# Performance work log

Measured on AMD Instinct MI355X. Metric: run time of the kernel, lower is better.

## Reference

```python
import jax, jax.numpy as jnp
import numpy as np

N, T, I_TEXT, H, P = 64, 1024, 512, 512, 256


def setup_inputs() -> dict:
    key = jax.random.key(0)
    ks = jax.random.split(key, 7)
    s = 0.05  # keep recurrent dynamics stable
    return {
        "text_encoding": jax.random.normal(ks[0], (N, T, I_TEXT), jnp.float32),
        "text_lengths": jnp.full((N,), T, dtype=jnp.int32),
        "W_ih": jax.random.normal(ks[1], (3 * H, I_TEXT + P), jnp.float32) * s,
        "W_hh": jax.random.normal(ks[2], (3 * H, H), jnp.float32) * s,
        "b_ih": jax.random.normal(ks[3], (3 * H,), jnp.float32) * s,
        "b_hh": jax.random.normal(ks[4], (3 * H,), jnp.float32) * s,
        "W_p": jax.random.normal(ks[5], (P, H), jnp.float32) * s,
        "b_p": jax.random.normal(ks[6], (P,), jnp.float32) * s,
    }


def reference(text_encoding, text_lengths, W_ih, W_hh, b_ih, b_hh, W_p, b_p):
    n, t, _ = text_encoding.shape
    h_dim = W_hh.shape[1]
    p_dim = W_p.shape[0]
    xs = jnp.transpose(text_encoding, (1, 0, 2))  # [T, N, I_text]

    def step(carry, x):
        h, prev = carry  # h: [N,H] GRU hidden, prev: [N,P] last projected prosody vec
        inp = jnp.concatenate([x, prev], axis=-1)          # [N, I_text+P]
        gi = inp @ W_ih.T + b_ih                           # [N, 3H]
        gh = h @ W_hh.T + b_hh                             # [N, 3H]
        i_r, i_z, i_n = jnp.split(gi, 3, axis=-1)
        h_r, h_z, h_n = jnp.split(gh, 3, axis=-1)
        r = jax.nn.sigmoid(i_r + h_r)
        z = jax.nn.sigmoid(i_z + h_z)
        g = jnp.tanh(i_n + r * h_n)
        h_new = (1.0 - z) * g + z * h
        pred = h_new @ W_p.T + b_p                         # [N, P]
        return (h_new, pred), pred

    h0 = jnp.zeros((n, h_dim), text_encoding.dtype)
    p0 = jnp.zeros((n, p_dim), text_encoding.dtype)
    _, preds = jax.lax.scan(step, (h0, p0), xs)            # [T, N, P]
    return jnp.transpose(preds, (1, 0, 2))                 # [N, T, P]
```

## Files before the change

kernel.cpp:

```cpp
#include <hip/hip_runtime.h>
#include <hip/hip_bf16.h>


typedef short short8 __attribute__((ext_vector_type(8)));
typedef float f32x4 __attribute__((ext_vector_type(4)));

__device__ __forceinline__ unsigned short f2bf(float f) {
  __hip_bfloat16 h = __float2bfloat16(f);
  return *reinterpret_cast<unsigned short*>(&h);
}

__global__ void k_zero(unsigned int* __restrict__ p, int n) {
  int i = blockIdx.x * 256 + threadIdx.x;
  if (i < n) p[i] = 0u;
}

__global__ void k_fold(const float* __restrict__ W_ih, const float* __restrict__ W_hh,
                       const float* __restrict__ W_p, const float* __restrict__ b_p,
                       float* __restrict__ W_big, float* __restrict__ v_bp) {
  int idx = blockIdx.x * 256 + threadIdx.x;
  int i = idx >> 9;
  int j = idx & 511;
  const float* wip = W_ih + (long)i * 768 + 512;
  float q = 0.f;
  for (int k = 0; k < 256; ++k) q = fmaf(wip[k], W_p[k * 512 + j], q);
  if (i < 1024) {
    W_big[(long)i * 512 + j] = W_hh[(long)i * 512 + j] + q;
  } else {
    W_big[(long)i * 512 + j] = q;
    W_big[(long)(i + 512) * 512 + j] = W_hh[(long)i * 512 + j];
  }
  if (j == 0) {
    float s = 0.f;
    for (int k = 0; k < 256; ++k) s = fmaf(b_p[k], wip[k], s);
    v_bp[i] = s;
  }
}

__global__ void k_pack(const float* __restrict__ W_big, const float* __restrict__ W_ih,
                       const float* __restrict__ W_p,
                       unsigned short* __restrict__ Wr, unsigned short* __restrict__ Wx) {
  long e = (long)blockIdx.x * 256 + threadIdx.x;
  if (e < 1572864) {
    int k = (int)(e & 511);
    int cc = (int)((e >> 9) & 15);
    int rest = (int)(e >> 13);
    int T = rest % 3, b = rest / 3;
    int j = b * 8 + (cc & 7);
    bool hi = cc >= 8;
    float v;
    if (T == 0)      v = W_big[(long)(hi ? 512 + j : j) * 512 + k];
    else if (T == 1) v = W_big[(long)(hi ? 1536 + j : 1024 + j) * 512 + k];
    else             v = (cc < 4) ? W_p[(long)(b * 4 + cc) * 512 + k] : 0.f;
    Wr[e] = f2bf(v);
  } else {
    long e2 = e - 1572864;
    int k = (int)(e2 & 511);
    int cc = (int)((e2 >> 9) & 15);
    int rest = (int)(e2 >> 13);
    int T = rest & 1, b = rest >> 1;
    float v = 0.f;
    if (T == 0) {
      int row = (cc < 8) ? (b * 8 + cc) : (512 + b * 8 + (cc - 8));
      v = W_ih[(long)row * 768 + k];
    } else if (cc < 8) {
      v = W_ih[(long)(1024 + b * 8 + cc) * 768 + k];
    }
    Wx[e2] = f2bf(v);
  }
}

__global__ __launch_bounds__(256, 1) void k_persist(
    const float* __restrict__ x,
    const unsigned short* __restrict__ Wr, const unsigned short* __restrict__ Wxr,
    const float* __restrict__ b_ih, const float* __restrict__ b_hh,
    const float* __restrict__ v_bp, const float* __restrict__ b_p,
    unsigned short* __restrict__ Hbf,
    float* __restrict__ out,
    unsigned int* __restrict__ flags,
    unsigned int* __restrict__ dead) {
  const int tid = threadIdx.x;
  const int b = blockIdx.x;
  const int w = tid >> 6, lane = tid & 63, c = lane & 15, q = lane >> 4;
  const int j0 = b * 8, n0 = w * 16, jj = j0 + (c & 7), pcol = b * 4 + (c & 3);

  __shared__ unsigned short wxl[32 * 528];

  short8 wr0[16], wr1[16], wr2[16];
#pragma unroll
  for (int ki = 0; ki < 16; ++ki) {
    wr0[ki] = *(const short8*)(Wr + (((long)(b * 3 + 0) * 16 + c) * 512 + ki * 32 + q * 8));
    wr1[ki] = *(const short8*)(Wr + (((long)(b * 3 + 1) * 16 + c) * 512 + ki * 32 + q * 8));
    wr2[ki] = *(const short8*)(Wr + (((long)(b * 3 + 2) * 16 + c) * 512 + ki * 32 + q * 8));
  }
  {
    const unsigned short* src = Wxr + (long)b * 16384;
    int row = tid >> 3, ch = tid & 7;
#pragma unroll
    for (int i = 0; i < 8; ++i) {
      int col = ch * 64 + i * 8;
      *(short8*)&wxl[row * 528 + col] = *(const short8*)(src + row * 512 + col);
    }
  }

  const float bihr = b_ih[jj],        bhhr = b_hh[jj],        vbr = v_bp[jj];
  const float bihz = b_ih[512 + jj],  bhhz = b_hh[512 + jj],  vbz = v_bp[512 + jj];
  const float bihn = b_ih[1024 + jj], bhhn = b_hh[1024 + jj], vbn = v_bp[1024 + jj];
  const float bp = b_p[pcol];
  float hprev[4] = {0.f, 0.f, 0.f, 0.f};
  f32x4 gp0{0.f, 0.f, 0.f, 0.f}, gp1 = gp0;
  bool alive = true;

  __syncthreads();

  auto produce = [&](int tt) {
    f32x4 p0{0.f, 0.f, 0.f, 0.f}, p1 = p0;
    const float* xr = x + ((long)(n0 + c) * 1024 + tt) * 512 + q * 8;
#pragma unroll
    for (int ki = 0; ki < 16; ++ki) {
      float4 f0 = *(const float4*)(xr + ki * 32);
      float4 f1 = *(const float4*)(xr + ki * 32 + 4);
      short8 ax;
      ax[0] = f2bf(f0.x); ax[1] = f2bf(f0.y); ax[2] = f2bf(f0.z); ax[3] = f2bf(f0.w);
      ax[4] = f2bf(f1.x); ax[5] = f2bf(f1.y); ax[6] = f2bf(f1.z); ax[7] = f2bf(f1.w);
      short8 b0 = *(const short8*)&wxl[c * 528 + ki * 32 + q * 8];
      short8 b1 = *(const short8*)&wxl[(16 + c) * 528 + ki * 32 + q * 8];
      p0 = __builtin_amdgcn_mfma_f32_16x16x32_bf16(ax, b0, p0, 0, 0, 0);
      p1 = __builtin_amdgcn_mfma_f32_16x16x32_bf16(ax, b1, p1, 0, 0, 0);
    }
    gp0 = p0; gp1 = p1;
  };

  produce(0);

  for (int t = 0; t <= 1024; ++t) {
    const int cur = t & 1;
    const unsigned short* hb = Hbf + (long)cur * 32768 + (long)(n0 + c) * 512 + q * 8;
    short8 h0, h1, h2, h3, h4, h5, h6, h7, h8, h9, hA, hB, hC, hD, hE, hF;
    asm volatile(
        "global_load_dwordx4 %[o0], %[a], off sc0 sc1\n\t"
        "global_load_dwordx4 %[o1], %[a], off offset:64 sc0 sc1\n\t"
        "global_load_dwordx4 %[o2], %[a], off offset:128 sc0 sc1\n\t"
        "global_load_dwordx4 %[o3], %[a], off offset:192 sc0 sc1\n\t"
        "global_load_dwordx4 %[o4], %[a], off offset:256 sc0 sc1\n\t"
        "global_load_dwordx4 %[o5], %[a], off offset:320 sc0 sc1\n\t"
        "global_load_dwordx4 %[o6], %[a], off offset:384 sc0 sc1\n\t"
        "global_load_dwordx4 %[o7], %[a], off offset:448 sc0 sc1\n\t"
        "global_load_dwordx4 %[o8], %[a], off offset:512 sc0 sc1\n\t"
        "global_load_dwordx4 %[o9], %[a], off offset:576 sc0 sc1\n\t"
        "global_load_dwordx4 %[oA], %[a], off offset:640 sc0 sc1\n\t"
        "global_load_dwordx4 %[oB], %[a], off offset:704 sc0 sc1\n\t"
        "global_load_dwordx4 %[oC], %[a], off offset:768 sc0 sc1\n\t"
        "global_load_dwordx4 %[oD], %[a], off offset:832 sc0 sc1\n\t"
        "global_load_dwordx4 %[oE], %[a], off offset:896 sc0 sc1\n\t"
        "global_load_dwordx4 %[oF], %[a], off offset:960 sc0 sc1\n\t"
        "s_waitcnt vmcnt(0)"
        : [o0]"=&v"(h0), [o1]"=&v"(h1), [o2]"=&v"(h2), [o3]"=&v"(h3),
          [o4]"=&v"(h4), [o5]"=&v"(h5), [o6]"=&v"(h6), [o7]"=&v"(h7),
          [o8]"=&v"(h8), [o9]"=&v"(h9), [oA]"=&v"(hA), [oB]"=&v"(hB),
          [oC]"=&v"(hC), [oD]"=&v"(hD), [oE]"=&v"(hE), [oF]"=&v"(hF)
        : [a]"v"(hb)
        : "memory");

    f32x4 a0{0.f, 0.f, 0.f, 0.f}, a1 = a0, a2 = a0;
#define RK(H, K)                                                          \
    a0 = __builtin_amdgcn_mfma_f32_16x16x32_bf16(H, wr0[K], a0, 0, 0, 0); \
    a1 = __builtin_amdgcn_mfma_f32_16x16x32_bf16(H, wr1[K], a1, 0, 0, 0); \
    a2 = __builtin_amdgcn_mfma_f32_16x16x32_bf16(H, wr2[K], a2, 0, 0, 0);
    RK(h0, 0)  RK(h1, 1)  RK(h2, 2)  RK(h3, 3)
    RK(h4, 4)  RK(h5, 5)  RK(h6, 6)  RK(h7, 7)
    RK(h8, 8)  RK(h9, 9)  RK(hA, 10) RK(hB, 11)
    RK(hC, 12) RK(hD, 13) RK(hE, 14) RK(hF, 15)
#undef RK

    if (t >= 1 && c < 4) {
#pragma unroll
      for (int r = 0; r < 4; ++r)
        out[((long)(n0 + q * 4 + r) * 1024 + (t - 1)) * 256 + pcol] = a2[r] + bp;
    }
    if (t == 1024) break;

    const float cR = t ? (bihr + bhhr + vbr) : (bihr + bhhr);
    const float cZ = t ? (bihz + bhhz + vbz) : (bihz + bhhz);
    const float cN = t ? (bihn + vbn) : bihn;
    float s0x[4], s1x[4];
#pragma unroll
    for (int r = 0; r < 4; ++r) { s0x[r] = a0[r] + gp0[r]; s1x[r] = a1[r] + gp1[r]; }
    unsigned short* hw = Hbf + (long)(cur ^ 1) * 32768 + (long)(n0 + q * 4) * 512 + jj;
#pragma unroll
    for (int r = 0; r < 4; ++r) {
      float ps0 = __shfl_xor(s0x[r], 8);
      float ps1 = __shfl_xor(s1x[r], 8);
      if (c < 8) {
        float rr = __builtin_amdgcn_rcpf(1.f + __expf(-(s0x[r] + cR)));
        float zz = __builtin_amdgcn_rcpf(1.f + __expf(-(ps0 + cZ)));
        float aa = s1x[r] + cN + rr * (ps1 + bhhn);
        float gg = 1.f - 2.f * __builtin_amdgcn_rcpf(1.f + __expf(2.f * aa));
        float hn = (1.f - zz) * gg + zz * hprev[r];
        hprev[r] = hn;
        unsigned short hv = f2bf(hn);
        unsigned short* pr = hw + r * 512;
        asm volatile("global_store_short %0, %1, off sc0 sc1" :: "v"(pr), "v"(hv) : "memory");
      }
    }

    asm volatile("s_waitcnt vmcnt(0)" ::: "memory");
    __syncthreads();
    const unsigned int rnd = (unsigned int)t + 1u;
    if (tid == 0 && alive)
      __hip_atomic_store(&flags[b * 16], rnd, __ATOMIC_RELAXED, __HIP_MEMORY_SCOPE_AGENT);

    if (t < 1023) produce(t + 1);

    if (tid < 64 && alive) {
      int spins = 0;
      while (__hip_atomic_load(&flags[tid * 16], __ATOMIC_RELAXED,
                               __HIP_MEMORY_SCOPE_AGENT) < rnd) {
        __builtin_amdgcn_s_sleep(1);
        if ((++spins & 2047) == 0) {
          if (__hip_atomic_load(dead, __ATOMIC_RELAXED, __HIP_MEMORY_SCOPE_AGENT)) {
            alive = false; break;
          }
          if (spins > 1000000) {
            __hip_atomic_store(dead, 1u, __ATOMIC_RELAXED, __HIP_MEMORY_SCOPE_AGENT);
            alive = false; break;
          }
        }
      }
    }
    __syncthreads();
  }
}

extern "C" void kernel_launch(void* const* d_in, const int* in_sizes, int n_in,
                              void* d_out, int out_size, void* d_ws, size_t ws_size,
                              hipStream_t stream) {
  const float* x    = (const float*)d_in[0];
  const float* W_ih = (const float*)d_in[2];
  const float* W_hh = (const float*)d_in[3];
  const float* b_ih = (const float*)d_in[4];
  const float* b_hh = (const float*)d_in[5];
  const float* W_p  = (const float*)d_in[6];
  const float* b_p  = (const float*)d_in[7];
  float* out = (float*)d_out;

  constexpr size_t OFF_WBIG = 0;
  constexpr size_t OFF_VBP  = 4194304;
  constexpr size_t OFF_WR   = 4202496;
  constexpr size_t OFF_WXR  = 7348224;
  constexpr size_t OFF_HBF  = 9445376;
  constexpr size_t OFF_FLG  = 9576448;
  constexpr size_t OFF_DEAD = 9580544;
  constexpr size_t WS_NEED  = 9580608;
  if (ws_size < WS_NEED) return;

  char* ws = (char*)d_ws;
  float* W_big        = (float*)(ws + OFF_WBIG);
  float* v_bp         = (float*)(ws + OFF_VBP);
  unsigned short* Wr  = (unsigned short*)(ws + OFF_WR);
  unsigned short* Wxr = (unsigned short*)(ws + OFF_WXR);
  unsigned short* Hbf = (unsigned short*)(ws + OFF_HBF);
  unsigned int* flags = (unsigned int*)(ws + OFF_FLG);
  unsigned int* dead  = (unsigned int*)(ws + OFF_DEAD);

  k_zero<<<133, 256, 0, stream>>>((unsigned int*)(ws + OFF_HBF), 33808);
  k_fold<<<3072, 256, 0, stream>>>(W_ih, W_hh, W_p, b_p, W_big, v_bp);
  k_pack<<<10240, 256, 0, stream>>>(W_big, W_ih, W_p, Wr, Wxr);
  k_persist<<<64, 256, 0, stream>>>(x, Wr, Wxr, b_ih, b_hh, v_bp, b_p,
                                    Hbf, out, flags, dead);
}
```

Baseline: 13.03 ms.

## Replace grid flag barrier with per-element step-tagged hidden state polling

The global barrier (block flag store, per-block spin on all flags, two __syncthreads) is removed. Each hidden-state element is now stored as a 32-bit word carrying the step number in its upper 16 bits next to the bf16 value. Consumers poll their own hidden-state loads until every tag matches the current step, then repack the words into bf16 MFMA operands. This drops barrier latency and lets blocks proceed as soon as their data is ready, at the cost of doubling hidden-state traffic, adding repacking work, and relying on ordering of the dword stores.

```diff
diff --git a/kernel.cpp b/kernel.cpp
--- a/kernel.cpp
+++ b/kernel.cpp
@@ -4,6 +4,7 @@
 
 typedef short short8 __attribute__((ext_vector_type(8)));
 typedef float f32x4 __attribute__((ext_vector_type(4)));
+typedef unsigned int u32x4 __attribute__((ext_vector_type(4)));
 
 __device__ __forceinline__ unsigned short f2bf(float f) {
   __hip_bfloat16 h = __float2bfloat16(f);
@@ -75,9 +76,8 @@
     const unsigned short* __restrict__ Wr, const unsigned short* __restrict__ Wxr,
     const float* __restrict__ b_ih, const float* __restrict__ b_hh,
     const float* __restrict__ v_bp, const float* __restrict__ b_p,
-    unsigned short* __restrict__ Hbf,
+    unsigned int* __restrict__ Hd,
     float* __restrict__ out,
-    unsigned int* __restrict__ flags,
     unsigned int* __restrict__ dead) {
   const int tid = threadIdx.x;
   const int b = blockIdx.x;
@@ -133,45 +133,81 @@
 
   produce(0);
 
+#define LOAD16(BASE)                                                        \
+  asm volatile(                                                             \
+      "global_load_dwordx4 %[o0], %[a], off sc0 sc1\n\t"                    \
+      "global_load_dwordx4 %[o1], %[a], off offset:16 sc0 sc1\n\t"          \
+      "global_load_dwordx4 %[o2], %[a], off offset:128 sc0 sc1\n\t"         \
+      "global_load_dwordx4 %[o3], %[a], off offset:144 sc0 sc1\n\t"         \
+      "global_load_dwordx4 %[o4], %[a], off offset:256 sc0 sc1\n\t"         \
+      "global_load_dwordx4 %[o5], %[a], off offset:272 sc0 sc1\n\t"         \
+      "global_load_dwordx4 %[o6], %[a], off offset:384 sc0 sc1\n\t"         \
+      "global_load_dwordx4 %[o7], %[a], off offset:400 sc0 sc1\n\t"         \
+      "global_load_dwordx4 %[o8], %[a], off offset:512 sc0 sc1\n\t"         \
+      "global_load_dwordx4 %[o9], %[a], off offset:528 sc0 sc1\n\t"         \
+      "global_load_dwordx4 %[oA], %[a], off offset:640 sc0 sc1\n\t"         \
+      "global_load_dwordx4 %[oB], %[a], off offset:656 sc0 sc1\n\t"         \
+      "global_load_dwordx4 %[oC], %[a], off offset:768 sc0 sc1\n\t"         \
+      "global_load_dwordx4 %[oD], %[a], off offset:784 sc0 sc1\n\t"         \
+      "global_load_dwordx4 %[oE], %[a], off offset:896 sc0 sc1\n\t"         \
+      "global_load_dwordx4 %[oF], %[a], off offset:912 sc0 sc1\n\t"         \
+      "s_waitcnt vmcnt(0)"                                                  \
+      : [o0]"=&v"(d0), [o1]"=&v"(d1), [o2]"=&v"(d2), [o3]"=&v"(d3),         \
+        [o4]"=&v"(d4), [o5]"=&v"(d5), [o6]"=&v"(d6), [o7]"=&v"(d7),         \
+        [o8]"=&v"(d8), [o9]"=&v"(d9), [oA]"=&v"(dA), [oB]"=&v"(dB),         \
+        [oC]"=&v"(dC), [oD]"=&v"(dD), [oE]"=&v"(dE), [oF]"=&v"(dF)          \
+      : [a]"v"(BASE)                                                        \
+      : "memory")
+
+#define ORT(DD) acc |= (DD.x ^ texp) | (DD.y ^ texp) | (DD.z ^ texp) | (DD.w ^ texp)
+
+#define POLL16(BASE)                                                        \
+  { int spins = 0;                                                          \
+    for (;;) {                                                              \
+      LOAD16(BASE);                                                         \
+      unsigned int acc = 0;                                                 \
+      ORT(d0); ORT(d1); ORT(d2); ORT(d3); ORT(d4); ORT(d5); ORT(d6); ORT(d7);\
+      ORT(d8); ORT(d9); ORT(dA); ORT(dB); ORT(dC); ORT(dD); ORT(dE); ORT(dF);\
+      if (!__any((int)(acc >> 16))) break;                                  \
+      if ((++spins & 63) == 0) {                                            \
+        if (__hip_atomic_load(dead, __ATOMIC_RELAXED, __HIP_MEMORY_SCOPE_AGENT)) { \
+          alive = false; break;                                             \
+        }                                                                   \
+        if (spins > 200000) {                                               \
+          __hip_atomic_store(dead, 1u, __ATOMIC_RELAXED, __HIP_MEMORY_SCOPE_AGENT); \
+          alive = false; break;                                             \
+        }                                                                   \
+      }                                                                     \
+    }                                                                       \
+  }
+
+#define PACK2(HI, LO) __builtin_amdgcn_perm((HI), (LO), 0x05040100u)
+#define PKMFMA(DA, DB, K)                                                   \
+  { u32x4 pw;                                                               \
+    pw.x = PACK2(DA.y, DA.x); pw.y = PACK2(DA.w, DA.z);                     \
+    pw.z = PACK2(DB.y, DB.x); pw.w = PACK2(DB.w, DB.z);                     \
+    short8 ah = __builtin_bit_cast(short8, pw);                             \
+    a0 = __builtin_amdgcn_mfma_f32_16x16x32_bf16(ah, wr0[K], a0, 0, 0, 0);  \
+    a1 = __builtin_amdgcn_mfma_f32_16x16x32_bf16(ah, wr1[K], a1, 0, 0, 0);  \
+    a2 = __builtin_amdgcn_mfma_f32_16x16x32_bf16(ah, wr2[K], a2, 0, 0, 0); }
+
   for (int t = 0; t <= 1024; ++t) {
     const int cur = t & 1;
-    const unsigned short* hb = Hbf + (long)cur * 32768 + (long)(n0 + c) * 512 + q * 8;
-    short8 h0, h1, h2, h3, h4, h5, h6, h7, h8, h9, hA, hB, hC, hD, hE, hF;
-    asm volatile(
-        "global_load_dwordx4 %[o0], %[a], off sc0 sc1\n\t"
-        "global_load_dwordx4 %[o1], %[a], off offset:64 sc0 sc1\n\t"
-        "global_load_dwordx4 %[o2], %[a], off offset:128 sc0 sc1\n\t"
-        "global_load_dwordx4 %[o3], %[a], off offset:192 sc0 sc1\n\t"
-        "global_load_dwordx4 %[o4], %[a], off offset:256 sc0 sc1\n\t"
-        "global_load_dwordx4 %[o5], %[a], off offset:320 sc0 sc1\n\t"
-        "global_load_dwordx4 %[o6], %[a], off offset:384 sc0 sc1\n\t"
-        "global_load_dwordx4 %[o7], %[a], off offset:448 sc0 sc1\n\t"
-        "global_load_dwordx4 %[o8], %[a], off offset:512 sc0 sc1\n\t"
-        "global_load_dwordx4 %[o9], %[a], off offset:576 sc0 sc1\n\t"
-        "global_load_dwordx4 %[oA], %[a], off offset:640 sc0 sc1\n\t"
-        "global_load_dwordx4 %[oB], %[a], off offset:704 sc0 sc1\n\t"
-        "global_load_dwordx4 %[oC], %[a], off offset:768 sc0 sc1\n\t"
-        "global_load_dwordx4 %[oD], %[a], off offset:832 sc0 sc1\n\t"
-        "global_load_dwordx4 %[oE], %[a], off offset:896 sc0 sc1\n\t"
-        "global_load_dwordx4 %[oF], %[a], off offset:960 sc0 sc1\n\t"
-        "s_waitcnt vmcnt(0)"
-        : [o0]"=&v"(h0), [o1]"=&v"(h1), [o2]"=&v"(h2), [o3]"=&v"(h3),
-          [o4]"=&v"(h4), [o5]"=&v"(h5), [o6]"=&v"(h6), [o7]"=&v"(h7),
-          [o8]"=&v"(h8), [o9]"=&v"(h9), [oA]"=&v"(hA), [oB]"=&v"(hB),
-          [oC]"=&v"(hC), [oD]"=&v"(hD), [oE]"=&v"(hE), [oF]"=&v"(hF)
-        : [a]"v"(hb)
-        : "memory");
+    const unsigned int texp = ((unsigned int)t) << 16;
+    const unsigned int* hp = Hd + (long)cur * 32768 + (long)(n0 + c) * 512 + q * 8;
 
     f32x4 a0{0.f, 0.f, 0.f, 0.f}, a1 = a0, a2 = a0;
-#define RK(H, K)                                                          \
-    a0 = __builtin_amdgcn_mfma_f32_16x16x32_bf16(H, wr0[K], a0, 0, 0, 0); \
-    a1 = __builtin_amdgcn_mfma_f32_16x16x32_bf16(H, wr1[K], a1, 0, 0, 0); \
-    a2 = __builtin_amdgcn_mfma_f32_16x16x32_bf16(H, wr2[K], a2, 0, 0, 0);
-    RK(h0, 0)  RK(h1, 1)  RK(h2, 2)  RK(h3, 3)
-    RK(h4, 4)  RK(h5, 5)  RK(h6, 6)  RK(h7, 7)
-    RK(h8, 8)  RK(h9, 9)  RK(hA, 10) RK(hB, 11)
-    RK(hC, 12) RK(hD, 13) RK(hE, 14) RK(hF, 15)
-#undef RK
+    u32x4 d0, d1, d2, d3, d4, d5, d6, d7, d8, d9, dA, dB, dC, dD, dE, dF;
+
+    POLL16(hp);
+    if (!alive) break;
+    PKMFMA(d0, d1, 0)  PKMFMA(d2, d3, 1)  PKMFMA(d4, d5, 2)  PKMFMA(d6, d7, 3)
+    PKMFMA(d8, d9, 4)  PKMFMA(dA, dB, 5)  PKMFMA(dC, dD, 6)  PKMFMA(dE, dF, 7)
+
+    POLL16(hp + 256);
+    if (!alive) break;
+    PKMFMA(d0, d1, 8)  PKMFMA(d2, d3, 9)  PKMFMA(d4, d5, 10) PKMFMA(d6, d7, 11)
+    PKMFMA(d8, d9, 12) PKMFMA(dA, dB, 13) PKMFMA(dC, dD, 14) PKMFMA(dE, dF, 15)
 
     if (t >= 1 && c < 4) {
 #pragma unroll
@@ -186,7 +222,8 @@
     float s0x[4], s1x[4];
 #pragma unroll
     for (int r = 0; r < 4; ++r) { s0x[r] = a0[r] + gp0[r]; s1x[r] = a1[r] + gp1[r]; }
-    unsigned short* hw = Hbf + (long)(cur ^ 1) * 32768 + (long)(n0 + q * 4) * 512 + jj;
+    unsigned int* hw = Hd + (long)(cur ^ 1) * 32768 + (long)(n0 + q * 4) * 512 + jj;
+    const unsigned int tg = ((unsigned int)(t + 1)) << 16;
 #pragma unroll
     for (int r = 0; r < 4; ++r) {
       float ps0 = __shfl_xor(s0x[r], 8);
@@ -198,38 +235,18 @@
         float gg = 1.f - 2.f * __builtin_amdgcn_rcpf(1.f + __expf(2.f * aa));
         float hn = (1.f - zz) * gg + zz * hprev[r];
         hprev[r] = hn;
-        unsigned short hv = f2bf(hn);
-        unsigned short* pr = hw + r * 512;
-        asm volatile("global_store_short %0, %1, off sc0 sc1" :: "v"(pr), "v"(hv) : "memory");
+        unsigned int hv = tg | (unsigned int)f2bf(hn);
+        const unsigned int* pr = hw + r * 512;
+        asm volatile("global_store_dword %0, %1, off sc0 sc1" :: "v"(pr), "v"(hv) : "memory");
       }
     }
-
-    asm volatile("s_waitcnt vmcnt(0)" ::: "memory");
-    __syncthreads();
-    const unsigned int rnd = (unsigned int)t + 1u;
-    if (tid == 0 && alive)
-      __hip_atomic_store(&flags[b * 16], rnd, __ATOMIC_RELAXED, __HIP_MEMORY_SCOPE_AGENT);
-
     if (t < 1023) produce(t + 1);
-
-    if (tid < 64 && alive) {
-      int spins = 0;
-      while (__hip_atomic_load(&flags[tid * 16], __ATOMIC_RELAXED,
-                               __HIP_MEMORY_SCOPE_AGENT) < rnd) {
-        __builtin_amdgcn_s_sleep(1);
-        if ((++spins & 2047) == 0) {
-          if (__hip_atomic_load(dead, __ATOMIC_RELAXED, __HIP_MEMORY_SCOPE_AGENT)) {
-            alive = false; break;
-          }
-          if (spins > 1000000) {
-            __hip_atomic_store(dead, 1u, __ATOMIC_RELAXED, __HIP_MEMORY_SCOPE_AGENT);
-            alive = false; break;
-          }
-        }
-      }
-    }
-    __syncthreads();
-  }
+  }
+#undef LOAD16
+#undef ORT
+#undef POLL16
+#undef PACK2
+#undef PKMFMA
 }
 
 extern "C" void kernel_launch(void* const* d_in, const int* in_sizes, int n_in,
@@ -248,10 +265,9 @@
   constexpr size_t OFF_VBP  = 4194304;
   constexpr size_t OFF_WR   = 4202496;
   constexpr size_t OFF_WXR  = 7348224;
-  constexpr size_t OFF_HBF  = 9445376;
-  constexpr size_t OFF_FLG  = 9576448;
-  constexpr size_t OFF_DEAD = 9580544;
-  constexpr size_t WS_NEED  = 9580608;
+  constexpr size_t OFF_HD   = 9445376;
+  constexpr size_t OFF_DEAD = 9707520;
+  constexpr size_t WS_NEED  = 9707584;
   if (ws_size < WS_NEED) return;
 
   char* ws = (char*)d_ws;
@@ -259,13 +275,12 @@
   float* v_bp         = (float*)(ws + OFF_VBP);
   unsigned short* Wr  = (unsigned short*)(ws + OFF_WR);
   unsigned short* Wxr = (unsigned short*)(ws + OFF_WXR);
-  unsigned short* Hbf = (unsigned short*)(ws + OFF_HBF);
-  unsigned int* flags = (unsigned int*)(ws + OFF_FLG);
+  unsigned int* Hd    = (unsigned int*)(ws + OFF_HD);
   unsigned int* dead  = (unsigned int*)(ws + OFF_DEAD);
 
-  k_zero<<<133, 256, 0, stream>>>((unsigned int*)(ws + OFF_HBF), 33808);
+  k_zero<<<257, 256, 0, stream>>>((unsigned int*)(ws + OFF_HD), 65552);
   k_fold<<<3072, 256, 0, stream>>>(W_ih, W_hh, W_p, b_p, W_big, v_bp);
   k_pack<<<10240, 256, 0, stream>>>(W_big, W_ih, W_p, Wr, Wxr);
   k_persist<<<64, 256, 0, stream>>>(x, Wr, Wxr, b_ih, b_hh, v_bp, b_p,
-                                    Hbf, out, flags, dead);
-}
+                                    Hd, out, dead);
+}
```

Result: faster. 12.67 ms (-2.7%).
